# Optimization experiments

Hardware: AMD Instinct MI355X
Metric: run time of the kernel (lower is better)

Reference implementation:

```python
import jax, jax.numpy as jnp
import numpy as np

LEVEL = 2
INV_SQRT2 = 0.7071067811865476
# subband order: index 0 is the approx (x_coeff1[0]); the 7 details match the
# {'aad','ada','add','daa','dad','dda','ddd'} dict keys of wavedec3 level-`LEVEL`.
SUBS = ['aaa', 'aad', 'ada', 'add', 'daa', 'dad', 'dda', 'ddd']


def dwt1(x, axis):
    # single-level Haar (db1, periodic) analysis along one axis
    x = jnp.moveaxis(x, axis, -1)
    n = x.shape[-1]
    x = x.reshape(*x.shape[:-1], n // 2, 2)
    a = (x[..., 0] + x[..., 1]) * INV_SQRT2
    d = (x[..., 0] - x[..., 1]) * INV_SQRT2
    return jnp.moveaxis(a, -1, axis), jnp.moveaxis(d, -1, axis)


def dwt3(x):
    # separable 3D Haar DWT over the last 3 axes -> 8 subbands keyed 'aaa'..'ddd'
    subs = {'': x}
    for axis in (-3, -2, -1):
        nxt = {}
        for k, v in subs.items():
            a, d = dwt1(v, axis)
            nxt[k + 'a'] = a
            nxt[k + 'd'] = d
        subs = nxt
    return subs


def idwt1(a, d, axis):
    a = jnp.moveaxis(a, axis, -1)
    d = jnp.moveaxis(d, axis, -1)
    x = jnp.stack([(a + d) * INV_SQRT2, (a - d) * INV_SQRT2], axis=-1)
    x = x.reshape(*x.shape[:-2], x.shape[-2] * 2)
    return jnp.moveaxis(x, -1, axis)


def idwt3(subs):
    for axis in (-1, -2, -3):
        prefixes = sorted(set(k[:-1] for k in subs))
        subs = {p: idwt1(subs[p + 'a'], subs[p + 'd'], axis) for p in prefixes}
    return subs['']


def upsample_zero_details(a):
    # one inverse-DWT level with all detail coeffs = 0 (finer levels are zeroed
    # in the original forward for jj in 2..level)
    for axis in (-3, -2, -1):
        a = jnp.repeat(a, 2, axis=axis) * INV_SQRT2
    return a


def setup_inputs() -> dict:
    key = jax.random.key(0)
    k1, k2, k3, k4 = jax.random.split(key, 4)
    B, C, D, H, W = 4, 32, 64, 64, 64
    m = D >> LEVEL  # 16 = modes1
    scale = 1.0 / (C * C)
    x_1 = jax.random.normal(k1, (B, C, D, H, W), dtype=jnp.float32)
    x_2 = jax.random.normal(k2, (B, C, D, H, W), dtype=jnp.float32)
    W1 = scale * jax.random.uniform(k3, (8, C, C, m, m, m), dtype=jnp.float32)
    W2 = scale * jax.random.uniform(k4, (8, C, C, m, m, m), dtype=jnp.float32)
    return {'x_1': x_1, 'x_2': x_2, 'W1': W1, 'W2': W2}


def reference(x_1, x_2, W1, W2):
    # batched wavelet decompose -> per-subband channel mixing of the coarsest
    # level (the only level the original transforms; finer details are zeroed)
    a1, a2 = x_1, x_2
    for _ in range(LEVEL):
        s1 = dwt3(a1)
        s2 = dwt3(a2)
        a1 = s1['aaa']
        a2 = s2['aaa']
    mixed = {}
    for idx, k in enumerate(SUBS):
        mixed[k] = (jnp.einsum('bixyz,ioxyz->boxyz', s1[k], W1[idx])
                    + jnp.einsum('bixyz,ioxyz->boxyz', s2[k], W2[idx]))
    x = idwt3(mixed)  # level LEVEL -> LEVEL-1
    for _ in range(LEVEL - 1):
        x = upsample_zero_details(x)
    return x
```

## Files before the change

### kernel.cpp

```cpp
#include <hip/hip_runtime.h>


#define M3 4096
#define KS 524288
#define IS 4194304

__global__ __launch_bounds__(256) void k_fwd(const float* __restrict__ x1,
                                             const float* __restrict__ x2,
                                             float* __restrict__ s) {
  const int tid = blockIdx.x * 256 + threadIdx.x;
  const int v    = tid & 4095;
  const int rest = tid >> 12;
  const int c   = rest & 31;
  const int b   = (rest >> 5) & 3;
  const int inp = rest >> 7;
  const float* __restrict__ X = inp ? x2 : x1;
  const int z = v & 15, y = (v >> 4) & 15, x = v >> 8;
  const float* base =
      X + ((((size_t)(b * 32 + c) * 64 + 4 * x) * 64 + 4 * y) * 64 + 4 * z);
  float blk[2][2][2] = {{{0.f, 0.f}, {0.f, 0.f}}, {{0.f, 0.f}, {0.f, 0.f}}};
#pragma unroll
  for (int dd = 0; dd < 4; ++dd) {
#pragma unroll
    for (int hh = 0; hh < 4; ++hh) {
      const float4 f = *reinterpret_cast<const float4*>(base + (dd * 64 + hh) * 64);
      blk[dd >> 1][hh >> 1][0] += f.x + f.y;
      blk[dd >> 1][hh >> 1][1] += f.z + f.w;
    }
  }
  const float a0 = blk[0][0][0], a1 = blk[0][0][1], a2 = blk[0][1][0], a3 = blk[0][1][1];
  const float a4 = blk[1][0][0], a5 = blk[1][0][1], a6 = blk[1][1][0], a7 = blk[1][1][1];
  const float t0 = a0 + a1, t1 = a0 - a1, t2 = a2 + a3, t3 = a2 - a3;
  const float t4 = a4 + a5, t5 = a4 - a5, t6 = a6 + a7, t7 = a6 - a7;
  const float u0 = t0 + t2, u2 = t0 - t2, u1 = t1 + t3, u3 = t1 - t3;
  const float u4 = t4 + t6, u6 = t4 - t6, u5 = t5 + t7, u7 = t5 - t7;
  float* o = s + (size_t)inp * IS + (size_t)(b * 32 + c) * M3 + v;
  o[0 * KS] = 0.125f * (u0 + u4);
  o[4 * KS] = 0.125f * (u0 - u4);
  o[1 * KS] = 0.125f * (u1 + u5);
  o[5 * KS] = 0.125f * (u1 - u5);
  o[2 * KS] = 0.125f * (u2 + u6);
  o[6 * KS] = 0.125f * (u2 - u6);
  o[3 * KS] = 0.125f * (u3 + u7);
  o[7 * KS] = 0.125f * (u3 - u7);
}

__global__ __launch_bounds__(256) void k_mix(const float* __restrict__ W1,
                                             const float* __restrict__ W2,
                                             const float* __restrict__ s,
                                             float* __restrict__ mixed) {
  const int bid  = blockIdx.x;
  const int k    = bid & 7;
  const int rest = bid >> 3;
  const int og   = rest & 3;
  const int vblk = rest >> 2;
  const int v = vblk * 256 + threadIdx.x;
  const float* pW1 = W1 + ((size_t)k * 1024 + og * 8) * M3 + v;
  const float* pW2 = W2 + ((size_t)k * 1024 + og * 8) * M3 + v;
  const float* ps  = s + (size_t)k * KS + v;
  float acc[4][8];
#pragma unroll
  for (int b = 0; b < 4; ++b)
#pragma unroll
    for (int oo = 0; oo < 8; ++oo) acc[b][oo] = 0.f;
#pragma unroll 2
  for (int i = 0; i < 32; ++i) {
    float s1b[4], s2b[4];
#pragma unroll
    for (int b = 0; b < 4; ++b) {
      s1b[b] = ps[(size_t)(b * 32 + i) * M3];
      s2b[b] = ps[(size_t)IS + (size_t)(b * 32 + i) * M3];
    }
#pragma unroll
    for (int oo = 0; oo < 8; ++oo) {
      const float w1 = pW1[(size_t)(i * 32 + oo) * M3];
      const float w2 = pW2[(size_t)(i * 32 + oo) * M3];
#pragma unroll
      for (int b = 0; b < 4; ++b) acc[b][oo] += s1b[b] * w1 + s2b[b] * w2;
    }
  }
  float* pm = mixed + (size_t)k * KS + (size_t)og * 8 * M3 + v;
#pragma unroll
  for (int b = 0; b < 4; ++b)
#pragma unroll
    for (int oo = 0; oo < 8; ++oo)
      pm[(size_t)b * (32 * M3) + (size_t)oo * M3] = acc[b][oo];
}

__global__ __launch_bounds__(256) void k_inv(const float* __restrict__ mixed,
                                             float* __restrict__ out) {
  const int tid = blockIdx.x * 256 + threadIdx.x;
  const int v = tid & 4095;
  const int o = (tid >> 12) & 31;
  const int b = tid >> 17;
  const float* pm = mixed + (size_t)(b * 32 + o) * M3 + v;
  const float m0 = pm[0 * (size_t)KS], m1 = pm[1 * (size_t)KS];
  const float m2 = pm[2 * (size_t)KS], m3 = pm[3 * (size_t)KS];
  const float m4 = pm[4 * (size_t)KS], m5 = pm[5 * (size_t)KS];
  const float m6 = pm[6 * (size_t)KS], m7 = pm[7 * (size_t)KS];
  const float t0 = m0 + m1, t1 = m0 - m1, t2 = m2 + m3, t3 = m2 - m3;
  const float t4 = m4 + m5, t5 = m4 - m5, t6 = m6 + m7, t7 = m6 - m7;
  const float u0 = t0 + t2, u2 = t0 - t2, u1 = t1 + t3, u3 = t1 - t3;
  const float u4 = t4 + t6, u6 = t4 - t6, u5 = t5 + t7, u7 = t5 - t7;
  float w[2][2][2];
  w[0][0][0] = 0.125f * (u0 + u4);
  w[1][0][0] = 0.125f * (u0 - u4);
  w[0][0][1] = 0.125f * (u1 + u5);
  w[1][0][1] = 0.125f * (u1 - u5);
  w[0][1][0] = 0.125f * (u2 + u6);
  w[1][1][0] = 0.125f * (u2 - u6);
  w[0][1][1] = 0.125f * (u3 + u7);
  w[1][1][1] = 0.125f * (u3 - u7);
  const int z = v & 15, y = (v >> 4) & 15, x = v >> 8;
  float* base =
      out + ((((size_t)(b * 32 + o) * 64 + 4 * x) * 64 + 4 * y) * 64 + 4 * z);
#pragma unroll
  for (int dd = 0; dd < 4; ++dd) {
    const int p = dd >> 1;
#pragma unroll
    for (int hh = 0; hh < 4; ++hh) {
      const int q = hh >> 1;
      const float lo = w[p][q][0], hi = w[p][q][1];
      float4 f;
      f.x = lo; f.y = lo; f.z = hi; f.w = hi;
      *reinterpret_cast<float4*>(base + (dd * 64 + hh) * 64) = f;
    }
  }
}

extern "C" void kernel_launch(void* const* d_in, const int* in_sizes, int n_in,
                              void* d_out, int out_size, void* d_ws, size_t ws_size,
                              hipStream_t stream) {
  const float* x1 = (const float*)d_in[0];
  const float* x2 = (const float*)d_in[1];
  const float* W1 = (const float*)d_in[2];
  const float* W2 = (const float*)d_in[3];
  float* out = (float*)d_out;
  float* s     = (float*)d_ws;
  float* mixed = s + 2 * (size_t)IS;
  k_fwd<<<4096, 256, 0, stream>>>(x1, x2, s);
  k_mix<<<512, 256, 0, stream>>>(W1, W2, s, mixed);
  k_inv<<<2048, 256, 0, stream>>>(mixed, out);
}
```

Measured before the change: 167.6 us.

## Stage forward DWT input slabs into LDS via direct global-to-LDS loads

The forward wavelet kernel now loads each contiguous 64KB x-slab into shared memory with global_load_lds, using an XOR swizzle to avoid bank conflicts. Threads then read float4s from LDS, and two half-blocks exchange partial sums through shared memory to finish the 8-subband butterfly. The goal is fully coalesced global reads, replacing the strided per-thread float4 reads of the old kernel. In exchange it uses 64KB+ of LDS per block, which limits occupancy, and it adds two barriers.

```diff
diff --git a/kernel.cpp b/kernel.cpp
--- a/kernel.cpp
+++ b/kernel.cpp
@@ -5,44 +5,78 @@
 #define KS 524288
 #define IS 4194304
 
-__global__ __launch_bounds__(256) void k_fwd(const float* __restrict__ x1,
-                                             const float* __restrict__ x2,
-                                             float* __restrict__ s) {
-  const int tid = blockIdx.x * 256 + threadIdx.x;
-  const int v    = tid & 4095;
-  const int rest = tid >> 12;
-  const int c   = rest & 31;
-  const int b   = (rest >> 5) & 3;
-  const int inp = rest >> 7;
-  const float* __restrict__ X = inp ? x2 : x1;
-  const int z = v & 15, y = (v >> 4) & 15, x = v >> 8;
-  const float* base =
-      X + ((((size_t)(b * 32 + c) * 64 + 4 * x) * 64 + 4 * y) * 64 + 4 * z);
-  float blk[2][2][2] = {{{0.f, 0.f}, {0.f, 0.f}}, {{0.f, 0.f}, {0.f, 0.f}}};
+__global__ __launch_bounds__(512, 4) void k_fwd(const float* __restrict__ x1,
+                                                const float* __restrict__ x2,
+                                                float* __restrict__ s) {
+  const int bid  = blockIdx.x;
+  const int xsl  = bid & 15;
+  const int rest = bid >> 4;
+  const int bc   = rest & 127;
+  const int inp  = rest >> 7;
+  const float* __restrict__ X =
+      (inp ? x2 : x1) + (size_t)bc * 262144 + (size_t)xsl * 16384;
+
+  __shared__ __align__(16) float slab[16384];
+  __shared__ __align__(16) float ex[2][256][4];
+
+  const int tid  = threadIdx.x;
+  const int lane = tid & 63;
+  const int wv   = tid >> 6;
+
 #pragma unroll
-  for (int dd = 0; dd < 4; ++dd) {
+  for (int r = 0; r < 8; ++r) {
+    const int cn = wv * 8 + r;
+    const int gslot = cn * 64 + (lane ^ ((cn & 3) << 1));
+    __builtin_amdgcn_global_load_lds(
+        (const __attribute__((address_space(1))) void*)(X + (size_t)gslot * 4),
+        (__attribute__((address_space(3))) void*)(&slab[cn * 256]),
+        16, 0, 0);
+  }
+  __syncthreads();
+
+  const int hf = tid >> 8;
+  const int v  = tid & 255;
+  const int z = v & 15, y = v >> 4;
+  float acc[2][2] = {{0.f, 0.f}, {0.f, 0.f}};
+#pragma unroll
+  for (int dp = 0; dp < 2; ++dp) {
+    const int dd = 2 * hf + dp;
 #pragma unroll
     for (int hh = 0; hh < 4; ++hh) {
-      const float4 f = *reinterpret_cast<const float4*>(base + (dd * 64 + hh) * 64);
-      blk[dd >> 1][hh >> 1][0] += f.x + f.y;
-      blk[dd >> 1][hh >> 1][1] += f.z + f.w;
+      const int row = dd * 64 + 4 * y + hh;
+      const int g   = row * 16 + z;
+      const int sp  = g ^ (((g >> 6) & 3) << 1);
+      const float4 f = *reinterpret_cast<const float4*>(&slab[sp * 4]);
+      acc[hh >> 1][0] += f.x + f.y;
+      acc[hh >> 1][1] += f.z + f.w;
     }
   }
-  const float a0 = blk[0][0][0], a1 = blk[0][0][1], a2 = blk[0][1][0], a3 = blk[0][1][1];
-  const float a4 = blk[1][0][0], a5 = blk[1][0][1], a6 = blk[1][1][0], a7 = blk[1][1][1];
+  float4 own;
+  own.x = acc[0][0]; own.y = acc[0][1]; own.z = acc[1][0]; own.w = acc[1][1];
+  *reinterpret_cast<float4*>(&ex[hf][v][0]) = own;
+  __syncthreads();
+  const float4 oth = *reinterpret_cast<const float4*>(&ex[hf ^ 1][v][0]);
+
+  const float a0 = hf ? oth.x : own.x, a1 = hf ? oth.y : own.y;
+  const float a2 = hf ? oth.z : own.z, a3 = hf ? oth.w : own.w;
+  const float a4 = hf ? own.x : oth.x, a5 = hf ? own.y : oth.y;
+  const float a6 = hf ? own.z : oth.z, a7 = hf ? own.w : oth.w;
   const float t0 = a0 + a1, t1 = a0 - a1, t2 = a2 + a3, t3 = a2 - a3;
   const float t4 = a4 + a5, t5 = a4 - a5, t6 = a6 + a7, t7 = a6 - a7;
   const float u0 = t0 + t2, u2 = t0 - t2, u1 = t1 + t3, u3 = t1 - t3;
   const float u4 = t4 + t6, u6 = t4 - t6, u5 = t5 + t7, u7 = t5 - t7;
-  float* o = s + (size_t)inp * IS + (size_t)(b * 32 + c) * M3 + v;
-  o[0 * KS] = 0.125f * (u0 + u4);
-  o[4 * KS] = 0.125f * (u0 - u4);
-  o[1 * KS] = 0.125f * (u1 + u5);
-  o[5 * KS] = 0.125f * (u1 - u5);
-  o[2 * KS] = 0.125f * (u2 + u6);
-  o[6 * KS] = 0.125f * (u2 - u6);
-  o[3 * KS] = 0.125f * (u3 + u7);
-  o[7 * KS] = 0.125f * (u3 - u7);
+  float* o = s + (size_t)inp * IS + (size_t)bc * M3 + xsl * 256 + y * 16 + z;
+  if (hf == 0) {
+    o[0 * KS] = 0.125f * (u0 + u4);
+    o[1 * KS] = 0.125f * (u1 + u5);
+    o[2 * KS] = 0.125f * (u2 + u6);
+    o[3 * KS] = 0.125f * (u3 + u7);
+  } else {
+    o[4 * KS] = 0.125f * (u0 - u4);
+    o[5 * KS] = 0.125f * (u1 - u5);
+    o[6 * KS] = 0.125f * (u2 - u6);
+    o[7 * KS] = 0.125f * (u3 - u7);
+  }
 }
 
 __global__ __launch_bounds__(256) void k_mix(const float* __restrict__ W1,
@@ -138,7 +172,7 @@
   float* out = (float*)d_out;
   float* s     = (float*)d_ws;
   float* mixed = s + 2 * (size_t)IS;
-  k_fwd<<<4096, 256, 0, stream>>>(x1, x2, s);
+  k_fwd<<<4096, 512, 0, stream>>>(x1, x2, s);
   k_mix<<<512, 256, 0, stream>>>(W1, W2, s, mixed);
   k_inv<<<2048, 256, 0, stream>>>(mixed, out);
 }
```

New measurement: 170.8 us. No clear change (+1.9%).

## Stream forward Haar input through double-buffered LDS via async global_load_lds

Applied to the files above, without the earlier changes.

The forward kernel now runs one block per (input, batch, channel) volume and walks it in 16 slabs of four depth planes each. Each slab is loaded asynchronously into a double-buffered, XOR-swizzled LDS buffer with global_load_lds, overlapping the next slab's load with reduction of the current one. This replaces many small, strided per-thread float4 global reads with fully coalesced bulk transfers. In exchange, the grid shrinks to 256 blocks of 512 threads, only half the threads compute, and the per-slab barriers with 128KB of LDS per block may limit occupancy.

```diff
diff --git a/kernel.cpp b/kernel.cpp
--- a/kernel.cpp
+++ b/kernel.cpp
@@ -4,45 +4,81 @@
 #define M3 4096
 #define KS 524288
 #define IS 4194304
+#define NSLAB 16
 
-__global__ __launch_bounds__(256) void k_fwd(const float* __restrict__ x1,
+__global__ __launch_bounds__(512) void k_fwd(const float* __restrict__ x1,
                                              const float* __restrict__ x2,
                                              float* __restrict__ s) {
-  const int tid = blockIdx.x * 256 + threadIdx.x;
-  const int v    = tid & 4095;
-  const int rest = tid >> 12;
-  const int c   = rest & 31;
-  const int b   = (rest >> 5) & 3;
-  const int inp = rest >> 7;
-  const float* __restrict__ X = inp ? x2 : x1;
-  const int z = v & 15, y = (v >> 4) & 15, x = v >> 8;
-  const float* base =
-      X + ((((size_t)(b * 32 + c) * 64 + 4 * x) * 64 + 4 * y) * 64 + 4 * z);
-  float blk[2][2][2] = {{{0.f, 0.f}, {0.f, 0.f}}, {{0.f, 0.f}, {0.f, 0.f}}};
+  const int blk = blockIdx.x;
+  const int bc  = blk & 127;
+  const int inp = blk >> 7;
+  const float* __restrict__ X = (inp ? x2 : x1) + (size_t)bc * 262144;
+
+  __shared__ __align__(16) float buf[2][16384];
+
+  const int tid  = threadIdx.x;
+  const int lane = tid & 63;
+  const int wv   = tid >> 6;
+
+  auto stage = [&](int xsl, int bi) {
 #pragma unroll
-  for (int dd = 0; dd < 4; ++dd) {
+    for (int r = 0; r < 8; ++r) {
+      const int cn = wv * 8 + r;
+      const int gslot = cn * 64 + (lane ^ ((cn & 3) << 1));
+      __builtin_amdgcn_global_load_lds(
+          (const __attribute__((address_space(1))) void*)(
+              X + (size_t)xsl * 16384 + (size_t)gslot * 4),
+          (__attribute__((address_space(3))) void*)(&buf[bi][cn * 256]),
+          16, 0, 0);
+    }
+  };
+
+  stage(0, 0);
+  for (int t = 0; t < NSLAB; ++t) {
+    if (t + 1 < NSLAB) {
+      stage(t + 1, (t + 1) & 1);
+      asm volatile("s_waitcnt vmcnt(8)" ::: "memory");
+    } else {
+      asm volatile("s_waitcnt vmcnt(0)" ::: "memory");
+    }
+    __builtin_amdgcn_s_barrier();
+    __builtin_amdgcn_sched_barrier(0);
+
+    if (tid < 256) {
+      const int z = tid & 15, y = tid >> 4;
+      const float* bp = buf[t & 1];
+      float acc[2][2][2] = {{{0.f, 0.f}, {0.f, 0.f}}, {{0.f, 0.f}, {0.f, 0.f}}};
 #pragma unroll
-    for (int hh = 0; hh < 4; ++hh) {
-      const float4 f = *reinterpret_cast<const float4*>(base + (dd * 64 + hh) * 64);
-      blk[dd >> 1][hh >> 1][0] += f.x + f.y;
-      blk[dd >> 1][hh >> 1][1] += f.z + f.w;
+      for (int dd = 0; dd < 4; ++dd) {
+#pragma unroll
+        for (int hh = 0; hh < 4; ++hh) {
+          const int row = dd * 64 + 4 * y + hh;
+          const int g   = row * 16 + z;
+          const int sp  = g ^ (((g >> 6) & 3) << 1);
+          const float4 f = *reinterpret_cast<const float4*>(&bp[sp * 4]);
+          acc[dd >> 1][hh >> 1][0] += f.x + f.y;
+          acc[dd >> 1][hh >> 1][1] += f.z + f.w;
+        }
+      }
+      const float a0 = acc[0][0][0], a1 = acc[0][0][1], a2 = acc[0][1][0], a3 = acc[0][1][1];
+      const float a4 = acc[1][0][0], a5 = acc[1][0][1], a6 = acc[1][1][0], a7 = acc[1][1][1];
+      const float t0 = a0 + a1, t1 = a0 - a1, t2 = a2 + a3, t3 = a2 - a3;
+      const float t4 = a4 + a5, t5 = a4 - a5, t6 = a6 + a7, t7 = a6 - a7;
+      const float u0 = t0 + t2, u2 = t0 - t2, u1 = t1 + t3, u3 = t1 - t3;
+      const float u4 = t4 + t6, u6 = t4 - t6, u5 = t5 + t7, u7 = t5 - t7;
+      float* o = s + (size_t)inp * IS + (size_t)bc * M3 + t * 256 + y * 16 + z;
+      o[0 * KS] = 0.125f * (u0 + u4);
+      o[4 * KS] = 0.125f * (u0 - u4);
+      o[1 * KS] = 0.125f * (u1 + u5);
+      o[5 * KS] = 0.125f * (u1 - u5);
+      o[2 * KS] = 0.125f * (u2 + u6);
+      o[6 * KS] = 0.125f * (u2 - u6);
+      o[3 * KS] = 0.125f * (u3 + u7);
+      o[7 * KS] = 0.125f * (u3 - u7);
     }
+    __builtin_amdgcn_sched_barrier(0);
+    __builtin_amdgcn_s_barrier();
   }
-  const float a0 = blk[0][0][0], a1 = blk[0][0][1], a2 = blk[0][1][0], a3 = blk[0][1][1];
-  const float a4 = blk[1][0][0], a5 = blk[1][0][1], a6 = blk[1][1][0], a7 = blk[1][1][1];
-  const float t0 = a0 + a1, t1 = a0 - a1, t2 = a2 + a3, t3 = a2 - a3;
-  const float t4 = a4 + a5, t5 = a4 - a5, t6 = a6 + a7, t7 = a6 - a7;
-  const float u0 = t0 + t2, u2 = t0 - t2, u1 = t1 + t3, u3 = t1 - t3;
-  const float u4 = t4 + t6, u6 = t4 - t6, u5 = t5 + t7, u7 = t5 - t7;
-  float* o = s + (size_t)inp * IS + (size_t)(b * 32 + c) * M3 + v;
-  o[0 * KS] = 0.125f * (u0 + u4);
-  o[4 * KS] = 0.125f * (u0 - u4);
-  o[1 * KS] = 0.125f * (u1 + u5);
-  o[5 * KS] = 0.125f * (u1 - u5);
-  o[2 * KS] = 0.125f * (u2 + u6);
-  o[6 * KS] = 0.125f * (u2 - u6);
-  o[3 * KS] = 0.125f * (u3 + u7);
-  o[7 * KS] = 0.125f * (u3 - u7);
 }
 
 __global__ __launch_bounds__(256) void k_mix(const float* __restrict__ W1,
@@ -138,7 +174,7 @@
   float* out = (float*)d_out;
   float* s     = (float*)d_ws;
   float* mixed = s + 2 * (size_t)IS;
-  k_fwd<<<4096, 256, 0, stream>>>(x1, x2, s);
+  k_fwd<<<256, 512, 0, stream>>>(x1, x2, s);
   k_mix<<<512, 256, 0, stream>>>(W1, W2, s, mixed);
   k_inv<<<2048, 256, 0, stream>>>(mixed, out);
 }
```

New measurement: 165.2 us. About the same (-1.4%).
